# Kernel tuning notes

Hardware: AMD Instinct MI355X
Metric: run time of the kernel (lower is better)

## Reference

```python
import jax, jax.numpy as jnp
import numpy as np

B, S, D = 4, 2048, 1024
H, HD = 16, 64  # num_head, head_dim


def setup_inputs() -> dict:
    key = jax.random.key(0)
    k0, k1, k2, k3, k4 = jax.random.split(key, 5)
    scale = 1.0 / np.sqrt(D)
    return {
        "x": jax.random.normal(k0, (B, S, D), dtype=jnp.float32),
        "Wq": jax.random.normal(k1, (D, H * HD), dtype=jnp.float32) * scale,
        "Wk": jax.random.normal(k2, (D, H * HD), dtype=jnp.float32) * scale,
        "Wv": jax.random.normal(k3, (D, H * HD), dtype=jnp.float32) * scale,
        "Wo": jax.random.normal(k4, (H * HD, H * HD), dtype=jnp.float32) * scale,
    }


def reference(x, Wq, Wk, Wv, Wo):
    b, s, _ = x.shape
    # projections -> [b, h, s, hd]
    q = (x @ Wq).reshape(b, s, H, HD).transpose(0, 2, 1, 3)
    k = (x @ Wk).reshape(b, s, H, HD).transpose(0, 2, 1, 3)
    v = (x @ Wv).reshape(b, s, H, HD).transpose(0, 2, 1, 3)
    # scaled scores [b, h, s, s]
    scores = jnp.einsum("bhqd,bhkd->bhqk", q, k) / np.sqrt(HD).astype(np.float32)
    causal = jnp.triu(jnp.ones((s, s), dtype=bool), k=1)  # True above diagonal
    scores = jnp.where(causal, -jnp.inf, scores)
    att = jax.nn.softmax(scores, axis=-1)
    # dropout p=0.0 -> identity
    out = jnp.einsum("bhqk,bhkd->bqhd", att, v).reshape(b, s, H * HD)
    return out @ Wo
```

## Files before the change

### kernel.cpp

```cpp
#include <hip/hip_runtime.h>


typedef __attribute__((ext_vector_type(8))) short short8_t;
typedef __attribute__((ext_vector_type(4))) short short4_t;
typedef __attribute__((ext_vector_type(4))) float float4_t;

constexpr int Bz = 4, Sq = 2048, Dm = 1024, NH = 16, HD = 64;

#define GLOAD_LDS16(g, l)                                                      \
  __builtin_amdgcn_global_load_lds(                                            \
      (const __attribute__((address_space(1))) unsigned int*)(g),              \
      (__attribute__((address_space(3))) unsigned int*)(l), 16, 0, 0)

__device__ __forceinline__ unsigned short f2bf(float f) {
  unsigned u = __builtin_bit_cast(unsigned, f);
  u += 0x7fffu + ((u >> 16) & 1u);
  return (unsigned short)(u >> 16);
}

__device__ __forceinline__ float exp2_fast(float x) {
#if __has_builtin(__builtin_amdgcn_exp2f)
  return __builtin_amdgcn_exp2f(x);
#else
  return exp2f(x);
#endif
}

__device__ __forceinline__ float m3(float a, float b, float c) {
  return fmaxf(fmaxf(a, b), c);
}

__global__ __launch_bounds__(256) void cast_x_kernel(const float* __restrict__ x,
                                                     unsigned short* __restrict__ xb) {
  size_t i = (size_t)blockIdx.x * 256 + threadIdx.x;
  float4 v = ((const float4*)x)[i];
  ushort4 o;
  o.x = f2bf(v.x); o.y = f2bf(v.y); o.z = f2bf(v.z); o.w = f2bf(v.w);
  ((ushort4*)xb)[i] = o;
}

__global__ __launch_bounds__(256) void transpose_w_kernel(
    const float* __restrict__ Wq, const float* __restrict__ Wk,
    const float* __restrict__ Wv, const float* __restrict__ Wo,
    unsigned short* __restrict__ wqT, unsigned short* __restrict__ wkT,
    unsigned short* __restrict__ wvT, unsigned short* __restrict__ woT) {
  __shared__ float tile[64][65];
  int zz = blockIdx.z;
  const float* W = zz == 0 ? Wq : (zz == 1 ? Wk : (zz == 2 ? Wv : Wo));
  unsigned short* WT = zz == 0 ? wqT : (zz == 1 ? wkT : (zz == 2 ? wvT : woT));
  int n0 = blockIdx.x * 64, k0 = blockIdx.y * 64;
  int tx = threadIdx.x & 63, ty = threadIdx.x >> 6;
#pragma unroll
  for (int i = 0; i < 16; ++i) {
    int r = i * 4 + ty;
    tile[r][tx] = W[(size_t)(k0 + r) * Dm + n0 + tx];
  }
  __syncthreads();
#pragma unroll
  for (int i = 0; i < 16; ++i) {
    int r = i * 4 + ty;
    WT[(size_t)(n0 + r) * Dm + k0 + tx] = f2bf(tile[tx][r]);
  }
}

__device__ __forceinline__ void gemm_mainloop(const unsigned short* __restrict__ A,
                                              const unsigned short* __restrict__ BT,
                                              int m0, int n0,
                                              unsigned short* lA, unsigned short* lB,
                                              float4_t acc[4][4]) {
  const int tid = threadIdx.x;
  const int lane = tid & 63, lr = lane & 15, quad = lane >> 4;
  const int wave = tid >> 6;
  const int mw = (wave >> 1) * 64, nw = (wave & 1) * 64;
  const int srow = tid >> 3;
  const int scol = (tid & 7) * 8;
  const unsigned short* ga = A + (size_t)(m0 + srow) * Dm + scol;
  const unsigned short* gb = BT + (size_t)(n0 + srow) * Dm + scol;
  unsigned short* la = lA + tid * 8;
  unsigned short* lb = lB + tid * 8;

  for (int k0 = 0; k0 < Dm; k0 += 64) {
    __syncthreads();
#pragma unroll
    for (int iss = 0; iss < 4; ++iss) {
      GLOAD_LDS16(ga + (size_t)iss * 32 * Dm + k0, la + iss * 32 * 64);
      GLOAD_LDS16(gb + (size_t)iss * 32 * Dm + k0, lb + iss * 32 * 64);
    }
    __syncthreads();
#pragma unroll
    for (int kk = 0; kk < 2; ++kk) {
      short8_t a[4], b[4];
#pragma unroll
      for (int i = 0; i < 4; ++i)
        a[i] = *(const short8_t*)(lA + (mw + i * 16 + lr) * 64 + kk * 32 + quad * 8);
#pragma unroll
      for (int j = 0; j < 4; ++j)
        b[j] = *(const short8_t*)(lB + (nw + j * 16 + lr) * 64 + kk * 32 + quad * 8);
#pragma unroll
      for (int i = 0; i < 4; ++i)
#pragma unroll
        for (int j = 0; j < 4; ++j)
          acc[i][j] = __builtin_amdgcn_mfma_f32_16x16x32_bf16(a[i], b[j], acc[i][j], 0, 0, 0);
    }
  }
}

__global__ __launch_bounds__(256) void gemm_qkv_kernel(
    const unsigned short* __restrict__ xb,
    const unsigned short* __restrict__ wqT, const unsigned short* __restrict__ wkT,
    const unsigned short* __restrict__ wvT,
    unsigned short* __restrict__ qb, unsigned short* __restrict__ kb,
    unsigned short* __restrict__ vt) {
  __shared__ unsigned short lA[128 * 64];
  __shared__ unsigned short lB[128 * 64];
  const unsigned short* WT = blockIdx.z == 0 ? wqT : (blockIdx.z == 1 ? wkT : wvT);
  unsigned short* outb = blockIdx.z == 0 ? qb : (blockIdx.z == 1 ? kb : vt);
  bool isV = blockIdx.z == 2;
  float qscale = (blockIdx.z == 0) ? 0.18033688011112042f : 1.0f;
  int lane = threadIdx.x & 63, wave = threadIdx.x >> 6;
  int lr = lane & 15, quad = lane >> 4;
  int m0 = blockIdx.y * 128, n0 = blockIdx.x * 128;
  int m_base = m0 + (wave >> 1) * 64;
  int n_base = n0 + (wave & 1) * 64;
  float4_t z = {0.f, 0.f, 0.f, 0.f};
  float4_t acc[4][4];
#pragma unroll
  for (int i = 0; i < 4; ++i)
#pragma unroll
    for (int j = 0; j < 4; ++j) acc[i][j] = z;
  gemm_mainloop(xb, WT, m0, n0, lA, lB, acc);
  if (isV) {
#pragma unroll
    for (int i = 0; i < 4; ++i)
#pragma unroll
      for (int j = 0; j < 4; ++j) {
        int m = m_base + i * 16 + quad * 4;
        int n = n_base + j * 16 + lr;
        int b = m >> 11, s = m & (Sq - 1);
        int h = n >> 6, hd = n & (HD - 1);
        ushort4 pk;
        pk.x = f2bf(acc[i][j][0]); pk.y = f2bf(acc[i][j][1]);
        pk.z = f2bf(acc[i][j][2]); pk.w = f2bf(acc[i][j][3]);
        *(ushort4*)(outb + (((size_t)b * NH + h) * HD + hd) * Sq + s) = pk;
      }
  } else {
#pragma unroll
    for (int i = 0; i < 4; ++i)
#pragma unroll
      for (int j = 0; j < 4; ++j)
#pragma unroll
        for (int r = 0; r < 4; ++r) {
          int m = m_base + i * 16 + quad * 4 + r;
          int n = n_base + j * 16 + lr;
          int b = m >> 11, s = m & (Sq - 1);
          int h = n >> 6, hd = n & (HD - 1);
          outb[(((size_t)b * NH + h) * Sq + s) * HD + hd] = f2bf(acc[i][j][r] * qscale);
        }
  }
}

__global__ __launch_bounds__(256) void gemm_out_kernel(
    const unsigned short* __restrict__ ao, const unsigned short* __restrict__ woT,
    float* __restrict__ out) {
  __shared__ unsigned short lA[128 * 64];
  __shared__ unsigned short lB[128 * 64];
  int lane = threadIdx.x & 63, wave = threadIdx.x >> 6;
  int lr = lane & 15, quad = lane >> 4;
  int m0 = blockIdx.y * 128, n0 = blockIdx.x * 128;
  int m_base = m0 + (wave >> 1) * 64;
  int n_base = n0 + (wave & 1) * 64;
  float4_t z = {0.f, 0.f, 0.f, 0.f};
  float4_t acc[4][4];
#pragma unroll
  for (int i = 0; i < 4; ++i)
#pragma unroll
    for (int j = 0; j < 4; ++j) acc[i][j] = z;
  gemm_mainloop(ao, woT, m0, n0, lA, lB, acc);
#pragma unroll
  for (int i = 0; i < 4; ++i)
#pragma unroll
    for (int j = 0; j < 4; ++j)
#pragma unroll
      for (int r = 0; r < 4; ++r) {
        int m = m_base + i * 16 + quad * 4 + r;
        int n = n_base + j * 16 + lr;
        out[(size_t)m * Dm + n] = acc[i][j][r];
      }
}

__global__ __launch_bounds__(256) void attn_kernel(
    const unsigned short* __restrict__ qbuf, const unsigned short* __restrict__ kbuf,
    const unsigned short* __restrict__ vtbuf, unsigned short* __restrict__ ao) {
  __shared__ unsigned short lk[2 * 64 * 64];
  __shared__ unsigned short lv[2 * 64 * 64];
  int tid = threadIdx.x;
  int bh = blockIdx.x;
  int ti = 31 - (int)blockIdx.y;
  int wave = tid >> 6, lane = tid & 63;
  int lcol = lane & 15, quad = lane >> 4;
  int lc7 = lcol & 7;
  const unsigned short* Q = qbuf + (size_t)bh * Sq * HD;
  const unsigned short* K = kbuf + (size_t)bh * Sq * HD;
  const unsigned short* Vt = vtbuf + (size_t)bh * HD * Sq;
  int b = bh >> 4, h = bh & 15;
  float4_t z = {0.f, 0.f, 0.f, 0.f};

  const int r0 = tid >> 3;
  const int sgk = (tid & 7) ^ (r0 & 7);
  const unsigned short* kg = K + (size_t)r0 * HD + sgk * 8;
  const int kdst = tid * 8;

  const int w0 = (tid & 7) * 2;
  const int xa = r0 & 15;
  const int d0 = w0 ^ xa;
  const unsigned short* vsrc = Vt + (size_t)r0 * Sq + w0 * 4;
  const int vdst = r0 * 64 + d0 * 4;

  const int koff0 = (quad ^ lc7) * 8;
  const int koff1 = ((quad | 4) ^ lc7) * 8;
  int voff[4];
#pragma unroll
  for (int s4 = 0; s4 < 4; ++s4) voff[s4] = ((s4 * 4 + quad) ^ lcol) * 4;

  unsigned short* lkc = lk;
  unsigned short* lkn = lk + 4096;
  unsigned short* lvc = lv;
  unsigned short* lvn = lv + 4096;

  int q0w = ti * 64 + wave * 16;
  int q_global = q0w + lcol;
  short8_t qf0 = *(const short8_t*)(Q + (size_t)(q0w + lcol) * HD + quad * 8);
  short8_t qf1 = *(const short8_t*)(Q + (size_t)(q0w + lcol) * HD + 32 + quad * 8);
  float m_i = -INFINITY, l_i = 0.f;
  float4_t o[4];
#pragma unroll
  for (int f = 0; f < 4; ++f) o[f] = z;

  {
    GLOAD_LDS16(kg, lkc + kdst);
    GLOAD_LDS16(kg + (size_t)32 * HD, lkc + 2048 + kdst);
    short4_t a0 = *(const short4_t*)(vsrc);
    short4_t a1 = *(const short4_t*)(vsrc + 4);
    short4_t b0 = *(const short4_t*)(vsrc + (size_t)32 * Sq);
    short4_t b1 = *(const short4_t*)(vsrc + (size_t)32 * Sq + 4);
    *(short4_t*)(lvc + vdst) = a0;
    *(short4_t*)(lvc + (vdst ^ 4)) = a1;
    *(short4_t*)(lvc + vdst + 2048) = b0;
    *(short4_t*)(lvc + (vdst ^ 4) + 2048) = b1;
  }
  __syncthreads();

  int nkt = ti + 1;
  for (int kt = 0; kt < nkt; ++kt) {
    bool has_next = (kt + 1 < nkt);
    short4_t a0, a1, b0, b1;
    if (has_next) {
      const unsigned short* vs = vsrc + (size_t)(kt + 1) * 64;
      a0 = *(const short4_t*)(vs);
      a1 = *(const short4_t*)(vs + 4);
      b0 = *(const short4_t*)(vs + (size_t)32 * Sq);
      b1 = *(const short4_t*)(vs + (size_t)32 * Sq + 4);
      const unsigned short* kgn = kg + (size_t)(kt + 1) * 64 * HD;
      GLOAD_LDS16(kgn, lkn + kdst);
      GLOAD_LDS16(kgn + (size_t)32 * HD, lkn + 2048 + kdst);
    }

    float s[16];
#pragma unroll
    for (int s4 = 0; s4 < 4; ++s4) {
      const unsigned short* kr = lkc + (s4 * 16 + lcol) * 64;
      short8_t kf0 = *(const short8_t*)(kr + koff0);
      short8_t kf1 = *(const short8_t*)(kr + koff1);
      float4_t st = z;
      st = __builtin_amdgcn_mfma_f32_16x16x32_bf16(kf0, qf0, st, 0, 0, 0);
      st = __builtin_amdgcn_mfma_f32_16x16x32_bf16(kf1, qf1, st, 0, 0, 0);
#pragma unroll
      for (int r = 0; r < 4; ++r) s[s4 * 4 + r] = st[r];
    }
    if (kt == ti) {
      int key0 = kt * 64;
#pragma unroll
      for (int s4 = 0; s4 < 4; ++s4)
#pragma unroll
        for (int r = 0; r < 4; ++r)
          if (key0 + s4 * 16 + quad * 4 + r > q_global) s[s4 * 4 + r] = -INFINITY;
    }

    float ta = m3(s[0], s[1], s[2]);
    float tb = m3(s[3], s[4], s[5]);
    float tc = m3(s[6], s[7], s[8]);
    float td = m3(s[9], s[10], s[11]);
    float te = m3(s[12], s[13], s[14]);
    float tmax = m3(ta, tb, tc);
    tmax = m3(tmax, td, te);
    tmax = fmaxf(tmax, s[15]);
    tmax = fmaxf(tmax, __shfl_xor(tmax, 16, 64));
    tmax = fmaxf(tmax, __shfl_xor(tmax, 32, 64));

    if (__any(tmax > m_i + 8.f)) {
      float m_new = fmaxf(m_i, tmax);
      float alpha = exp2_fast(m_i - m_new);
      l_i *= alpha;
      m_i = m_new;
      float at[4];
#pragma unroll
      for (int r = 0; r < 4; ++r) at[r] = __shfl(alpha, quad * 4 + r, 64);
#pragma unroll
      for (int f = 0; f < 4; ++f)
#pragma unroll
        for (int r = 0; r < 4; ++r) o[f][r] *= at[r];
    }

    float psum = 0.f;
    short4_t pf[4];
#pragma unroll
    for (int s4 = 0; s4 < 4; ++s4) {
      float p0 = exp2_fast(s[s4 * 4 + 0] - m_i);
      float p1 = exp2_fast(s[s4 * 4 + 1] - m_i);
      float p2 = exp2_fast(s[s4 * 4 + 2] - m_i);
      float p3 = exp2_fast(s[s4 * 4 + 3] - m_i);
      psum += (p0 + p1) + (p2 + p3);
      unsigned lo, hi;
      asm("v_cvt_pk_bf16_f32 %0, %1, %2" : "=v"(lo) : "v"(p0), "v"(p1));
      asm("v_cvt_pk_bf16_f32 %0, %1, %2" : "=v"(hi) : "v"(p2), "v"(p3));
      uint2 packed;
      packed.x = lo;
      packed.y = hi;
      pf[s4] = __builtin_bit_cast(short4_t, packed);
    }
    psum += __shfl_xor(psum, 16, 64);
    psum += __shfl_xor(psum, 32, 64);
    l_i += psum;

    if (has_next) {
      *(short4_t*)(lvn + vdst) = a0;
      *(short4_t*)(lvn + (vdst ^ 4)) = a1;
      *(short4_t*)(lvn + vdst + 2048) = b0;
      *(short4_t*)(lvn + (vdst ^ 4) + 2048) = b1;
    }

#pragma unroll
    for (int f = 0; f < 4; ++f) {
      const unsigned short* vr = lvc + (f * 16 + lcol) * 64;
#pragma unroll
      for (int s4 = 0; s4 < 4; ++s4) {
        short4_t vf = *(const short4_t*)(vr + voff[s4]);
        o[f] = __builtin_amdgcn_mfma_f32_16x16x16bf16_1k(pf[s4], vf, o[f], 0, 0, 0);
      }
    }

    __syncthreads();
    unsigned short* t;
    t = lkc; lkc = lkn; lkn = t;
    t = lvc; lvc = lvn; lvn = t;
  }

  float lt[4];
#pragma unroll
  for (int r = 0; r < 4; ++r) lt[r] = 1.f / __shfl(l_i, quad * 4 + r, 64);
#pragma unroll
  for (int f = 0; f < 4; ++f)
#pragma unroll
    for (int r = 0; r < 4; ++r) {
      int q = q0w + quad * 4 + r;
      int hd = f * 16 + lcol;
      ao[((size_t)b * Sq + q) * (NH * HD) + h * HD + hd] = f2bf(o[f][r] * lt[r]);
    }
}

extern "C" void kernel_launch(void* const* d_in, const int* in_sizes, int n_in,
                              void* d_out, int out_size, void* d_ws, size_t ws_size,
                              hipStream_t stream) {
  const float* x = (const float*)d_in[0];
  const float* Wq = (const float*)d_in[1];
  const float* Wk = (const float*)d_in[2];
  const float* Wv = (const float*)d_in[3];
  const float* Wo = (const float*)d_in[4];
  float* out = (float*)d_out;

  char* ws = (char*)d_ws;
  size_t off = 0;
  auto carve = [&](size_t bytes) {
    void* p = ws + off;
    off += (bytes + 255) & ~(size_t)255;
    return p;
  };
  const size_t xe = (size_t)Bz * Sq * Dm;
  const size_t we = (size_t)Dm * Dm;
  unsigned short* xb = (unsigned short*)carve(xe * 2);
  unsigned short* wqT = (unsigned short*)carve(we * 2);
  unsigned short* wkT = (unsigned short*)carve(we * 2);
  unsigned short* wvT = (unsigned short*)carve(we * 2);
  unsigned short* woT = (unsigned short*)carve(we * 2);
  unsigned short* qb = (unsigned short*)carve(xe * 2);
  unsigned short* kb = (unsigned short*)carve(xe * 2);
  unsigned short* vt = (unsigned short*)carve(xe * 2);
  unsigned short* ao = (unsigned short*)carve(xe * 2);
  (void)ws_size;

  cast_x_kernel<<<xe / 4 / 256, 256, 0, stream>>>(x, xb);
  transpose_w_kernel<<<dim3(16, 16, 4), 256, 0, stream>>>(Wq, Wk, Wv, Wo,
                                                          wqT, wkT, wvT, woT);
  gemm_qkv_kernel<<<dim3(8, 64, 3), 256, 0, stream>>>(xb, wqT, wkT, wvT, qb, kb, vt);
  attn_kernel<<<dim3(Bz * NH, 32), 256, 0, stream>>>(qb, kb, vt, ao);
  gemm_out_kernel<<<dim3(8, 64), 256, 0, stream>>>(ao, woT, out);
}
```

Baseline: 270.4 us.

## Rewrite projection GEMMs as 256x256 double-buffered, swizzled, interleaved-schedule kernels

Replaces the 128x128 single-buffered GEMM mainloop with a 256x256 tile, 8-wave kernel. It double-buffers LDS through global_load_lds, uses an XOR-swizzled LDS layout to avoid bank conflicts, and interleaves staged loads with MFMA groups behind explicit barriers and waitcnts. It also remaps the block index so that neighbouring blocks share operand tiles. The aim is to hide global-load latency, raise data reuse per block and improve L2 locality. In exchange it uses 128KB of LDS per block and more registers, and the QKV and output GEMMs launch only 384 and 128 blocks, which may underfill the GPU.

```diff
diff --git a/kernel.cpp b/kernel.cpp
--- a/kernel.cpp
+++ b/kernel.cpp
@@ -63,128 +63,186 @@
   }
 }
 
-__device__ __forceinline__ void gemm_mainloop(const unsigned short* __restrict__ A,
-                                              const unsigned short* __restrict__ BT,
-                                              int m0, int n0,
-                                              unsigned short* lA, unsigned short* lB,
-                                              float4_t acc[4][4]) {
+#define SBAR do { __builtin_amdgcn_sched_barrier(0); __builtin_amdgcn_s_barrier(); } while (0)
+#define VMW(n_) asm volatile("s_waitcnt vmcnt(" #n_ ")" ::: "memory")
+
+#define STG_A(buf_, h_, kt_) do {                                              \
+  GLOAD_LDS16(gA + (size_t)(mloc0 + (h_) * 64) * Dm + (kt_) * 64 + csA,        \
+              smA + (buf_) * 16384 + (h_) * 8192 + tid * 8);                   \
+  GLOAD_LDS16(gA + (size_t)(mloc1 + (h_) * 64) * Dm + (kt_) * 64 + csA,        \
+              smA + (buf_) * 16384 + (h_) * 8192 + 4096 + tid * 8);            \
+} while (0)
+#define STG_B(buf_, h_, kt_) do {                                              \
+  GLOAD_LDS16(gB + (size_t)(nloc0 + (h_) * 32) * Dm + (kt_) * 64 + csA,        \
+              smB + (buf_) * 16384 + (h_) * 8192 + tid * 8);                   \
+  GLOAD_LDS16(gB + (size_t)(nloc1 + (h_) * 32) * Dm + (kt_) * 64 + csA,        \
+              smB + (buf_) * 16384 + (h_) * 8192 + 4096 + tid * 8);            \
+} while (0)
+#define LDA_(buf_, mh_) do {                                                   \
+  _Pragma("unroll") for (int i_ = 0; i_ < 4; ++i_) {                           \
+    const unsigned short* p_ = smA + (buf_) * 16384 + (mh_) * 8192 + aoff + i_ * 1024; \
+    a[i_][0] = *(const short8_t*)(p_ + csw0);                                  \
+    a[i_][1] = *(const short8_t*)(p_ + csw1);                                  \
+  }                                                                            \
+} while (0)
+#define LDB_(dst_, buf_, nh_) do {                                             \
+  _Pragma("unroll") for (int j_ = 0; j_ < 2; ++j_) {                           \
+    const unsigned short* p_ = smB + (buf_) * 16384 + (nh_) * 8192 + boff + j_ * 1024; \
+    dst_[j_][0] = *(const short8_t*)(p_ + csw0);                               \
+    dst_[j_][1] = *(const short8_t*)(p_ + csw1);                               \
+  }                                                                            \
+} while (0)
+#define MF_(ioff_, breg_, joff_) do {                                          \
+  __builtin_amdgcn_s_setprio(1);                                               \
+  _Pragma("unroll") for (int i_ = 0; i_ < 4; ++i_)                             \
+  _Pragma("unroll") for (int j_ = 0; j_ < 2; ++j_) {                           \
+    acc[(ioff_) + i_][(joff_) + j_] = __builtin_amdgcn_mfma_f32_16x16x32_bf16( \
+        a[i_][0], breg_[j_][0], acc[(ioff_) + i_][(joff_) + j_], 0, 0, 0);     \
+    acc[(ioff_) + i_][(joff_) + j_] = __builtin_amdgcn_mfma_f32_16x16x32_bf16( \
+        a[i_][1], breg_[j_][1], acc[(ioff_) + i_][(joff_) + j_], 0, 0, 0);     \
+  }                                                                            \
+  __builtin_amdgcn_s_setprio(0);                                               \
+} while (0)
+
+__device__ __forceinline__ void gemm256_mainloop(
+    const unsigned short* __restrict__ A, const unsigned short* __restrict__ BT,
+    int m0, int n0, unsigned short* smA, unsigned short* smB,
+    float4_t acc[8][4]) {
   const int tid = threadIdx.x;
   const int lane = tid & 63, lr = lane & 15, quad = lane >> 4;
-  const int wave = tid >> 6;
-  const int mw = (wave >> 1) * 64, nw = (wave & 1) * 64;
-  const int srow = tid >> 3;
-  const int scol = (tid & 7) * 8;
-  const unsigned short* ga = A + (size_t)(m0 + srow) * Dm + scol;
-  const unsigned short* gb = BT + (size_t)(n0 + srow) * Dm + scol;
-  unsigned short* la = lA + tid * 8;
-  unsigned short* lb = lB + tid * 8;
-
-  for (int k0 = 0; k0 < Dm; k0 += 64) {
-    __syncthreads();
-#pragma unroll
-    for (int iss = 0; iss < 4; ++iss) {
-      GLOAD_LDS16(ga + (size_t)iss * 32 * Dm + k0, la + iss * 32 * 64);
-      GLOAD_LDS16(gb + (size_t)iss * 32 * Dm + k0, lb + iss * 32 * 64);
-    }
-    __syncthreads();
-#pragma unroll
-    for (int kk = 0; kk < 2; ++kk) {
-      short8_t a[4], b[4];
-#pragma unroll
-      for (int i = 0; i < 4; ++i)
-        a[i] = *(const short8_t*)(lA + (mw + i * 16 + lr) * 64 + kk * 32 + quad * 8);
-#pragma unroll
-      for (int j = 0; j < 4; ++j)
-        b[j] = *(const short8_t*)(lB + (nw + j * 16 + lr) * 64 + kk * 32 + quad * 8);
-#pragma unroll
-      for (int i = 0; i < 4; ++i)
-#pragma unroll
-        for (int j = 0; j < 4; ++j)
-          acc[i][j] = __builtin_amdgcn_mfma_f32_16x16x32_bf16(a[i], b[j], acc[i][j], 0, 0, 0);
-    }
-  }
-}
-
-__global__ __launch_bounds__(256) void gemm_qkv_kernel(
+  const int wid = tid >> 6, wm = wid >> 2, wn = wid & 3;
+  const int aoff = (wm * 64 + lr) * 64;
+  const int boff = (wn * 32 + lr) * 64;
+  const int csw0 = (quad ^ (lr & 7)) * 8;
+  const int csw1 = csw0 ^ 32;
+  const int lrow0 = tid >> 3;
+  const int csA = ((tid & 7) ^ (lrow0 & 7)) * 8;
+  const int mloc0 = lrow0, mloc1 = lrow0 + 128;
+  const int nloc0 = (lrow0 >> 5) * 64 + (lrow0 & 31);
+  const int nloc1 = nloc0 + 128;
+  const unsigned short* gA = A + (size_t)m0 * Dm;
+  const unsigned short* gB = BT + (size_t)n0 * Dm;
+
+  short8_t a[4][2], b0[2][2], b1[2][2];
+
+  STG_A(0, 0, 0); STG_A(0, 1, 0); STG_B(0, 0, 0); STG_B(0, 1, 0);
+  STG_A(1, 0, 1); STG_B(1, 0, 1); STG_B(1, 1, 1);
+  VMW(6);
+  SBAR;
+
+#pragma unroll 1
+  for (int T = 0; T < 7; ++T) {
+    const int t1 = 2 * T + 1, t2 = 2 * T + 2, t3 = 2 * T + 3;
+    LDA_(0, 0); LDB_(b0, 0, 0); STG_A(1, 1, t1); SBAR; MF_(0, b0, 0); SBAR;
+    LDB_(b1, 0, 1);             STG_A(0, 0, t2); SBAR; MF_(0, b1, 2); SBAR;
+    LDA_(0, 1);                 STG_B(0, 0, t2); SBAR; MF_(4, b0, 0); SBAR;
+                                STG_B(0, 1, t2); SBAR; MF_(4, b1, 2); VMW(6); SBAR;
+    LDA_(1, 0); LDB_(b0, 1, 0); STG_A(0, 1, t2); SBAR; MF_(0, b0, 0); SBAR;
+    LDB_(b1, 1, 1);             STG_A(1, 0, t3); SBAR; MF_(0, b1, 2); SBAR;
+    LDA_(1, 1);                 STG_B(1, 0, t3); SBAR; MF_(4, b0, 0); SBAR;
+                                STG_B(1, 1, t3); SBAR; MF_(4, b1, 2); VMW(6); SBAR;
+  }
+  LDA_(0, 0); LDB_(b0, 0, 0); STG_A(1, 1, 15); SBAR; MF_(0, b0, 0); SBAR;
+  LDB_(b1, 0, 1);                              SBAR; MF_(0, b1, 2); SBAR;
+  LDA_(0, 1);                                  SBAR; MF_(4, b0, 0); SBAR;
+                                               SBAR; MF_(4, b1, 2); VMW(0); SBAR;
+  LDA_(1, 0); LDB_(b0, 1, 0);                  SBAR; MF_(0, b0, 0); SBAR;
+  LDB_(b1, 1, 1);                              SBAR; MF_(0, b1, 2); SBAR;
+  LDA_(1, 1);                                  SBAR; MF_(4, b0, 0); SBAR;
+                                               SBAR; MF_(4, b1, 2);
+}
+
+__global__ __launch_bounds__(512, 2) void gemm_qkv_kernel(
     const unsigned short* __restrict__ xb,
     const unsigned short* __restrict__ wqT, const unsigned short* __restrict__ wkT,
     const unsigned short* __restrict__ wvT,
     unsigned short* __restrict__ qb, unsigned short* __restrict__ kb,
     unsigned short* __restrict__ vt) {
-  __shared__ unsigned short lA[128 * 64];
-  __shared__ unsigned short lB[128 * 64];
-  const unsigned short* WT = blockIdx.z == 0 ? wqT : (blockIdx.z == 1 ? wkT : wvT);
-  unsigned short* outb = blockIdx.z == 0 ? qb : (blockIdx.z == 1 ? kb : vt);
-  bool isV = blockIdx.z == 2;
-  float qscale = (blockIdx.z == 0) ? 0.18033688011112042f : 1.0f;
-  int lane = threadIdx.x & 63, wave = threadIdx.x >> 6;
-  int lr = lane & 15, quad = lane >> 4;
-  int m0 = blockIdx.y * 128, n0 = blockIdx.x * 128;
-  int m_base = m0 + (wave >> 1) * 64;
-  int n_base = n0 + (wave & 1) * 64;
+  __shared__ unsigned short smA[32768];
+  __shared__ unsigned short smB[32768];
+  int lin = (int)blockIdx.x;
+  int logical = (lin & 7) * 48 + (lin >> 3);
+  int bx = logical & 3;
+  int by = (logical >> 2) & 31;
+  int bz = logical >> 7;
+  const unsigned short* WT = bz == 0 ? wqT : (bz == 1 ? wkT : wvT);
+  unsigned short* outb = bz == 0 ? qb : (bz == 1 ? kb : vt);
+  bool isV = bz == 2;
+  float qscale = (bz == 0) ? 0.18033688011112042f : 1.0f;
+  int m0 = by * 256, n0 = bx * 256;
   float4_t z = {0.f, 0.f, 0.f, 0.f};
-  float4_t acc[4][4];
-#pragma unroll
-  for (int i = 0; i < 4; ++i)
+  float4_t acc[8][4];
+#pragma unroll
+  for (int i = 0; i < 8; ++i)
 #pragma unroll
     for (int j = 0; j < 4; ++j) acc[i][j] = z;
-  gemm_mainloop(xb, WT, m0, n0, lA, lB, acc);
+  gemm256_mainloop(xb, WT, m0, n0, smA, smB, acc);
+
+  const int lane = threadIdx.x & 63, lr = lane & 15, quad = lane >> 4;
+  const int wid = threadIdx.x >> 6, wm = wid >> 2, wn = wid & 3;
+  const int mb = m0 + wm * 128 + quad * 4;
+  const int nb = n0 + wn * 64 + lr;
   if (isV) {
 #pragma unroll
-    for (int i = 0; i < 4; ++i)
-#pragma unroll
-      for (int j = 0; j < 4; ++j) {
-        int m = m_base + i * 16 + quad * 4;
-        int n = n_base + j * 16 + lr;
+    for (int ai = 0; ai < 8; ++ai)
+#pragma unroll
+      for (int bj = 0; bj < 4; ++bj) {
+        int m = mb + (ai >> 2) * 64 + (ai & 3) * 16;
+        int n = nb + (bj >> 1) * 32 + (bj & 1) * 16;
         int b = m >> 11, s = m & (Sq - 1);
         int h = n >> 6, hd = n & (HD - 1);
         ushort4 pk;
-        pk.x = f2bf(acc[i][j][0]); pk.y = f2bf(acc[i][j][1]);
-        pk.z = f2bf(acc[i][j][2]); pk.w = f2bf(acc[i][j][3]);
+        pk.x = f2bf(acc[ai][bj][0]); pk.y = f2bf(acc[ai][bj][1]);
+        pk.z = f2bf(acc[ai][bj][2]); pk.w = f2bf(acc[ai][bj][3]);
         *(ushort4*)(outb + (((size_t)b * NH + h) * HD + hd) * Sq + s) = pk;
       }
   } else {
 #pragma unroll
-    for (int i = 0; i < 4; ++i)
-#pragma unroll
-      for (int j = 0; j < 4; ++j)
+    for (int ai = 0; ai < 8; ++ai)
+#pragma unroll
+      for (int bj = 0; bj < 4; ++bj)
 #pragma unroll
         for (int r = 0; r < 4; ++r) {
-          int m = m_base + i * 16 + quad * 4 + r;
-          int n = n_base + j * 16 + lr;
+          int m = mb + (ai >> 2) * 64 + (ai & 3) * 16 + r;
+          int n = nb + (bj >> 1) * 32 + (bj & 1) * 16;
           int b = m >> 11, s = m & (Sq - 1);
           int h = n >> 6, hd = n & (HD - 1);
-          outb[(((size_t)b * NH + h) * Sq + s) * HD + hd] = f2bf(acc[i][j][r] * qscale);
+          outb[(((size_t)b * NH + h) * Sq + s) * HD + hd] = f2bf(acc[ai][bj][r] * qscale);
         }
   }
 }
 
-__global__ __launch_bounds__(256) void gemm_out_kernel(
+__global__ __launch_bounds__(512, 2) void gemm_out_kernel(
     const unsigned short* __restrict__ ao, const unsigned short* __restrict__ woT,
     float* __restrict__ out) {
-  __shared__ unsigned short lA[128 * 64];
-  __shared__ unsigned short lB[128 * 64];
-  int lane = threadIdx.x & 63, wave = threadIdx.x >> 6;
-  int lr = lane & 15, quad = lane >> 4;
-  int m0 = blockIdx.y * 128, n0 = blockIdx.x * 128;
-  int m_base = m0 + (wave >> 1) * 64;
-  int n_base = n0 + (wave & 1) * 64;
+  __shared__ unsigned short smA[32768];
+  __shared__ unsigned short smB[32768];
+  int lin = (int)blockIdx.x;
+  int logical = (lin & 7) * 16 + (lin >> 3);
+  int bx = logical & 3;
+  int by = logical >> 2;
+  int m0 = by * 256, n0 = bx * 256;
   float4_t z = {0.f, 0.f, 0.f, 0.f};
-  float4_t acc[4][4];
-#pragma unroll
-  for (int i = 0; i < 4; ++i)
+  float4_t acc[8][4];
+#pragma unroll
+  for (int i = 0; i < 8; ++i)
 #pragma unroll
     for (int j = 0; j < 4; ++j) acc[i][j] = z;
-  gemm_mainloop(ao, woT, m0, n0, lA, lB, acc);
-#pragma unroll
-  for (int i = 0; i < 4; ++i)
-#pragma unroll
-    for (int j = 0; j < 4; ++j)
+  gemm256_mainloop(ao, woT, m0, n0, smA, smB, acc);
+
+  const int lane = threadIdx.x & 63, lr = lane & 15, quad = lane >> 4;
+  const int wid = threadIdx.x >> 6, wm = wid >> 2, wn = wid & 3;
+  const int mb = m0 + wm * 128 + quad * 4;
+  const int nb = n0 + wn * 64 + lr;
+#pragma unroll
+  for (int ai = 0; ai < 8; ++ai)
+#pragma unroll
+    for (int bj = 0; bj < 4; ++bj)
 #pragma unroll
       for (int r = 0; r < 4; ++r) {
-        int m = m_base + i * 16 + quad * 4 + r;
-        int n = n_base + j * 16 + lr;
-        out[(size_t)m * Dm + n] = acc[i][j][r];
+        int m = mb + (ai >> 2) * 64 + (ai & 3) * 16 + r;
+        int n = nb + (bj >> 1) * 32 + (bj & 1) * 16;
+        out[(size_t)m * Dm + n] = acc[ai][bj][r];
       }
 }
 
@@ -401,7 +459,7 @@
   cast_x_kernel<<<xe / 4 / 256, 256, 0, stream>>>(x, xb);
   transpose_w_kernel<<<dim3(16, 16, 4), 256, 0, stream>>>(Wq, Wk, Wv, Wo,
                                                           wqT, wkT, wvT, woT);
-  gemm_qkv_kernel<<<dim3(8, 64, 3), 256, 0, stream>>>(xb, wqT, wkT, wvT, qb, kb, vt);
+  gemm_qkv_kernel<<<384, 512, 0, stream>>>(xb, wqT, wkT, wvT, qb, kb, vt);
   attn_kernel<<<dim3(Bz * NH, 32), 256, 0, stream>>>(qb, kb, vt, ao);
-  gemm_out_kernel<<<dim3(8, 64), 256, 0, stream>>>(ao, woT, out);
-}
+  gemm_out_kernel<<<128, 512, 0, stream>>>(ao, woT, out);
+}
```

Result: faster. 262.8 us (-2.8%).
